# Kernel tuning notes

Hardware: AMD Instinct MI355X
Metric: run time of the kernel (lower is better)

## Reference

```python
import jax, jax.numpy as jnp
import numpy as np

N_ENT = 100000
EMBED_DIM = 128
N_EDGES = 3200000
SPARSE_THRESHOLD = 5


def setup_inputs() -> dict:
    key = jax.random.key(0)
    k1, k2, k3, k4 = jax.random.split(key, 4)
    entity_embeds = jax.random.normal(k1, (N_ENT, EMBED_DIM), dtype=jnp.float32)
    node_degrees = jax.random.randint(k2, (N_ENT,), 0, 40, dtype=jnp.int64)
    path_rows = jnp.sort(jax.random.randint(k3, (N_EDGES,), 0, N_ENT, dtype=jnp.int64))
    path_cols = jax.random.randint(k4, (N_EDGES,), 0, N_ENT, dtype=jnp.int64)
    return {
        "entity_embeds": entity_embeds,
        "node_degrees": node_degrees,
        "path_rows": path_rows,
        "path_cols": path_cols,
    }


def reference(entity_embeds, node_degrees, path_rows, path_cols):
    N, dim = entity_embeds.shape
    # node_edge_count = scatter_add(ones, rows), clamped to >= 1
    ones = jnp.ones(path_rows.shape[0], dtype=entity_embeds.dtype)
    node_edge_count = jax.ops.segment_sum(ones, path_rows, num_segments=N)
    node_edge_count = jnp.clip(node_edge_count, 1.0, None)
    # SpMM: remote[i] = sum over path edges (i -> j) of entity_embeds[j]
    gathered = entity_embeds[path_cols]  # [E, dim] (fused into segment_sum by XLA)
    remote = jax.ops.segment_sum(gathered, path_rows, num_segments=N)
    # degree-normalize then mask to sparse (low-degree) nodes only
    remote = remote / node_edge_count[:, None]
    sparse_mask = (node_degrees <= SPARSE_THRESHOLD).astype(entity_embeds.dtype)
    remote = remote * sparse_mask[:, None]
    return remote
```

## Files before the change

kernel.cpp:

```cpp
#include <hip/hip_runtime.h>

#define N_ENT 100000
#define EMBED_DIM 128
#define SPARSE_THRESHOLD 5

__global__ __launch_bounds__(EMBED_DIM) void path_agg_kernel(
    const float* __restrict__ embeds,
    const int*   __restrict__ degrees,
    const int*   __restrict__ rows,
    const int*   __restrict__ cols,
    float*       __restrict__ out,
    int n_edges)
{
    const int row = blockIdx.x;
    const int t   = threadIdx.x;
    float* orow = out + (size_t)row * EMBED_DIM;

    if (degrees[row] > SPARSE_THRESHOLD) {
        orow[t] = 0.0f;
        return;
    }

    int lo = 0, hi = n_edges;
    while (lo < hi) {
        int mid = (lo + hi) >> 1;
        if (rows[mid] < row) lo = mid + 1; else hi = mid;
    }
    const int start = lo;
    hi = n_edges;
    while (lo < hi) {
        int mid = (lo + hi) >> 1;
        if (rows[mid] <= row) lo = mid + 1; else hi = mid;
    }
    const int end = lo;

    float acc = 0.0f;
    int e = start;
    for (; e + 3 < end; e += 4) {
        int c0 = cols[e + 0];
        int c1 = cols[e + 1];
        int c2 = cols[e + 2];
        int c3 = cols[e + 3];
        float v0 = embeds[(size_t)c0 * EMBED_DIM + t];
        float v1 = embeds[(size_t)c1 * EMBED_DIM + t];
        float v2 = embeds[(size_t)c2 * EMBED_DIM + t];
        float v3 = embeds[(size_t)c3 * EMBED_DIM + t];
        acc += v0; acc += v1; acc += v2; acc += v3;
    }
    for (; e < end; ++e) {
        int c = cols[e];
        acc += embeds[(size_t)c * EMBED_DIM + t];
    }

    const int cnt = end - start;
    const float inv = 1.0f / (float)(cnt > 0 ? cnt : 1);
    orow[t] = acc * inv;
}

extern "C" void kernel_launch(void* const* d_in, const int* in_sizes, int n_in,
                              void* d_out, int out_size, void* d_ws, size_t ws_size,
                              hipStream_t stream) {
    const float* embeds  = (const float*)d_in[0];
    const int*   degrees = (const int*)d_in[1];
    const int*   rows    = (const int*)d_in[2];
    const int*   cols    = (const int*)d_in[3];
    float* out = (float*)d_out;
    const int n_edges = in_sizes[2];

    path_agg_kernel<<<N_ENT, EMBED_DIM, 0, stream>>>(
        embeds, degrees, rows, cols, out, n_edges);
}
```

Baseline: 191.7 us.

## Build CSR row offsets in a pre-pass and vectorize gather with float4

Adds a pre-pass kernel that computes per-row start offsets from the sorted row array, replacing the two global binary searches each block did over 3.2M edges. The main kernel now packs 8 rows per 256-thread block, with 32 lanes per row each loading float4, to cut per-block overhead and use wider loads. It adds a second launch and needs workspace, falling back to the old binary-search kernel if the workspace is too small.

```diff
diff --git a/kernel.cpp b/kernel.cpp
--- a/kernel.cpp
+++ b/kernel.cpp
@@ -3,8 +3,73 @@
 #define N_ENT 100000
 #define EMBED_DIM 128
 #define SPARSE_THRESHOLD 5
+#define ROWS_PER_BLOCK 8
 
-__global__ __launch_bounds__(EMBED_DIM) void path_agg_kernel(
+__global__ void seg_bounds_kernel(const int* __restrict__ rows,
+                                  int* __restrict__ row_start,
+                                  int n_edges) {
+    int e = blockIdx.x * blockDim.x + threadIdx.x;
+    const int stride = gridDim.x * blockDim.x;
+    for (; e < n_edges; e += stride) {
+        const int r  = rows[e];
+        const int rp = (e == 0) ? -1 : rows[e - 1];
+        for (int q = rp + 1; q <= r; ++q) row_start[q] = e;
+        if (e == n_edges - 1) {
+            for (int q = r + 1; q <= N_ENT; ++q) row_start[q] = n_edges;
+        }
+    }
+}
+
+__global__ __launch_bounds__(256) void path_agg_kernel(
+    const float4* __restrict__ embeds4,
+    const int*    __restrict__ degrees,
+    const int*    __restrict__ row_start,
+    const int*    __restrict__ cols,
+    float4*       __restrict__ out4)
+{
+    const int sub  = threadIdx.x >> 5;
+    const int lane = threadIdx.x & 31;
+    const int row  = blockIdx.x * ROWS_PER_BLOCK + sub;
+
+    float4* orow = out4 + (size_t)row * 32;
+
+    if (degrees[row] > SPARSE_THRESHOLD) {
+        orow[lane] = make_float4(0.f, 0.f, 0.f, 0.f);
+        return;
+    }
+
+    const int start = row_start[row];
+    const int end   = row_start[row + 1];
+
+    float4 acc = make_float4(0.f, 0.f, 0.f, 0.f);
+    int e = start;
+    for (; e + 4 <= end; e += 4) {
+        const int c0 = cols[e + 0];
+        const int c1 = cols[e + 1];
+        const int c2 = cols[e + 2];
+        const int c3 = cols[e + 3];
+        float4 v0 = embeds4[(size_t)c0 * 32 + lane];
+        float4 v1 = embeds4[(size_t)c1 * 32 + lane];
+        float4 v2 = embeds4[(size_t)c2 * 32 + lane];
+        float4 v3 = embeds4[(size_t)c3 * 32 + lane];
+        acc.x += v0.x; acc.y += v0.y; acc.z += v0.z; acc.w += v0.w;
+        acc.x += v1.x; acc.y += v1.y; acc.z += v1.z; acc.w += v1.w;
+        acc.x += v2.x; acc.y += v2.y; acc.z += v2.z; acc.w += v2.w;
+        acc.x += v3.x; acc.y += v3.y; acc.z += v3.z; acc.w += v3.w;
+    }
+    for (; e < end; ++e) {
+        const int c = cols[e];
+        float4 v = embeds4[(size_t)c * 32 + lane];
+        acc.x += v.x; acc.y += v.y; acc.z += v.z; acc.w += v.w;
+    }
+
+    const int cnt = end - start;
+    const float inv = 1.0f / (float)(cnt > 0 ? cnt : 1);
+    acc.x *= inv; acc.y *= inv; acc.z *= inv; acc.w *= inv;
+    orow[lane] = acc;
+}
+
+__global__ __launch_bounds__(EMBED_DIM) void path_agg_bsearch_kernel(
     const float* __restrict__ embeds,
     const int*   __restrict__ degrees,
     const int*   __restrict__ rows,
@@ -16,45 +81,21 @@
     const int t   = threadIdx.x;
     float* orow = out + (size_t)row * EMBED_DIM;
 
-    if (degrees[row] > SPARSE_THRESHOLD) {
-        orow[t] = 0.0f;
-        return;
-    }
+    if (degrees[row] > SPARSE_THRESHOLD) { orow[t] = 0.0f; return; }
 
     int lo = 0, hi = n_edges;
-    while (lo < hi) {
-        int mid = (lo + hi) >> 1;
-        if (rows[mid] < row) lo = mid + 1; else hi = mid;
-    }
+    while (lo < hi) { int mid = (lo + hi) >> 1; if (rows[mid] < row) lo = mid + 1; else hi = mid; }
     const int start = lo;
     hi = n_edges;
-    while (lo < hi) {
-        int mid = (lo + hi) >> 1;
-        if (rows[mid] <= row) lo = mid + 1; else hi = mid;
-    }
+    while (lo < hi) { int mid = (lo + hi) >> 1; if (rows[mid] <= row) lo = mid + 1; else hi = mid; }
     const int end = lo;
 
     float acc = 0.0f;
-    int e = start;
-    for (; e + 3 < end; e += 4) {
-        int c0 = cols[e + 0];
-        int c1 = cols[e + 1];
-        int c2 = cols[e + 2];
-        int c3 = cols[e + 3];
-        float v0 = embeds[(size_t)c0 * EMBED_DIM + t];
-        float v1 = embeds[(size_t)c1 * EMBED_DIM + t];
-        float v2 = embeds[(size_t)c2 * EMBED_DIM + t];
-        float v3 = embeds[(size_t)c3 * EMBED_DIM + t];
-        acc += v0; acc += v1; acc += v2; acc += v3;
-    }
-    for (; e < end; ++e) {
-        int c = cols[e];
-        acc += embeds[(size_t)c * EMBED_DIM + t];
-    }
+    for (int e = start; e < end; ++e)
+        acc += embeds[(size_t)cols[e] * EMBED_DIM + t];
 
     const int cnt = end - start;
-    const float inv = 1.0f / (float)(cnt > 0 ? cnt : 1);
-    orow[t] = acc * inv;
+    orow[t] = acc / (float)(cnt > 0 ? cnt : 1);
 }
 
 extern "C" void kernel_launch(void* const* d_in, const int* in_sizes, int n_in,
@@ -67,6 +108,14 @@
     float* out = (float*)d_out;
     const int n_edges = in_sizes[2];
 
-    path_agg_kernel<<<N_ENT, EMBED_DIM, 0, stream>>>(
-        embeds, degrees, rows, cols, out, n_edges);
+    const size_t needed = (size_t)(N_ENT + 1) * sizeof(int);
+    if (ws_size >= needed) {
+        int* row_start = (int*)d_ws;
+        seg_bounds_kernel<<<1024, 256, 0, stream>>>(rows, row_start, n_edges);
+        path_agg_kernel<<<N_ENT / ROWS_PER_BLOCK, 256, 0, stream>>>(
+            (const float4*)embeds, degrees, row_start, cols, (float4*)out);
+    } else {
+        path_agg_bsearch_kernel<<<N_ENT, EMBED_DIM, 0, stream>>>(
+            embeds, degrees, rows, cols, out, n_edges);
+    }
 }
```

New measurement: 155.6 us. -18.8%, faster.
